# Kernel optimization log

Measured on AMD Instinct MI355X. Metric: run time of the kernel, lower is better.

## Reference

```python
import jax, jax.numpy as jnp
import numpy as np

B, T, D = 512, 200, 512

def setup_inputs() -> dict:
    key = jax.random.key(0)
    k1, k2, k3 = jax.random.split(key, 3)
    inputs = jax.random.normal(k1, (B, T, D), dtype=jnp.float32)
    # Keras 'uniform' initializer -> U(-0.05, 0.05)
    W = jax.random.uniform(k2, (T, T), minval=-0.05, maxval=0.05, dtype=jnp.float32)
    b = jax.random.uniform(k3, (T,), minval=-0.05, maxval=0.05, dtype=jnp.float32)
    return {"inputs": inputs, "W": W, "b": b}

def reference(inputs, W, b):
    # x = permute(inputs, (0,2,1)) -> [B, D, T]; scores over timestep axis
    # a = softmax(tanh(x @ W + b)) along last axis (T)
    scores = jnp.tanh(jnp.einsum('btd,ts->bds', inputs, W) + b)  # [B, D, T]
    a = jax.nn.softmax(scores, axis=-1)                           # softmax over T
    # permute back to [B, T, D], elementwise multiply, sum over T -> [B, D]
    out = jnp.einsum('bdt,btd->bd', a, inputs)
    return out
```

## Files before the change

### kernel.cpp

```cpp
#include <hip/hip_runtime.h>
#include <cstdint>
#include <cstddef>

#define B_DIM 512
#define T_DIM 200
#define D_DIM 512
#define NPAD  208
#define NKG   28
#define NT    13
#define KS_STEPS 7

typedef short  short8  __attribute__((ext_vector_type(8)));
typedef float  floatx4 __attribute__((ext_vector_type(4)));

__device__ __forceinline__ unsigned short f2bf(float f) {
  unsigned int u = __float_as_uint(f);
  u += 0x7fffu + ((u >> 16) & 1u);
  return (unsigned short)(u >> 16);
}
__device__ __forceinline__ float bf2f(unsigned short h) {
  return __uint_as_float(((unsigned int)h) << 16);
}

__global__ void prep_w_kernel(const float* __restrict__ W,
                              unsigned short* __restrict__ wf) {
  int idx = blockIdx.x * blockDim.x + threadIdx.x;
  if (idx >= NKG * 8 * NPAD) return;
  int k = idx / NPAD;
  int n = idx - k * NPAD;
  float v = (k < T_DIM && n < T_DIM) ? W[k * T_DIM + n] : 0.0f;
  wf[((size_t)(k >> 3) * NPAD + n) * 8 + (k & 7)] = f2bf(v);
}

__global__ __launch_bounds__(256, 4)
void attn_kernel(const float* __restrict__ X,
                 const unsigned short* __restrict__ wf,
                 const float* __restrict__ bias,
                 float* __restrict__ out) {
  __shared__ __align__(16) unsigned short Xa[4 * NKG * 16 * 8];

  const int tid  = threadIdx.x;
  const int wv   = tid >> 6;
  const int lane = tid & 63;
  const int l15  = lane & 15;
  const int g    = lane >> 4;

  const int gw = blockIdx.x * 4 + wv;
  const int bb = gw >> 5;
  const int d0 = (gw & 31) << 4;

  unsigned short* Xw = Xa + wv * (NKG * 16 * 8);
  const float* xbase = X + (size_t)bb * T_DIM * D_DIM + d0 + l15;

  float cur[8], nxt[8];
  {
    const float* p = xbase + (size_t)(g * 8) * D_DIM;
    #pragma unroll
    for (int j = 0; j < 8; ++j) cur[j] = p[(size_t)j * D_DIM];
  }
  #pragma unroll
  for (int ks = 0; ks < KS_STEPS; ++ks) {
    if (ks < 6) {
      if (ks < 5 || g == 0) {
        const float* p = xbase + (size_t)((ks + 1) * 32 + g * 8) * D_DIM;
        #pragma unroll
        for (int j = 0; j < 8; ++j) nxt[j] = p[(size_t)j * D_DIM];
      } else {
        #pragma unroll
        for (int j = 0; j < 8; ++j) nxt[j] = 0.0f;
      }
    }
    int4 w;
    w.x = (int)f2bf(cur[0]) | ((int)f2bf(cur[1]) << 16);
    w.y = (int)f2bf(cur[2]) | ((int)f2bf(cur[3]) << 16);
    w.z = (int)f2bf(cur[4]) | ((int)f2bf(cur[5]) << 16);
    w.w = (int)f2bf(cur[6]) | ((int)f2bf(cur[7]) << 16);
    *(int4*)&Xw[(((ks * 4 + g) * 16) + l15) * 8] = w;
    #pragma unroll
    for (int j = 0; j < 8; ++j) cur[j] = nxt[j];
  }

  floatx4 acc[NT];
  #pragma unroll
  for (int nt = 0; nt < NT; ++nt)
    acc[nt] = (floatx4){0.f, 0.f, 0.f, 0.f};

  #pragma unroll
  for (int ks = 0; ks < KS_STEPS; ++ks) {
    const int kg = ks * 4 + g;
    short8 a = *(const short8*)&Xw[((kg * 16) + l15) * 8];
    const unsigned short* wp = wf + ((size_t)kg * NPAD + l15) * 8;
    #pragma unroll
    for (int nt = 0; nt < NT; ++nt) {
      short8 bfr = *(const short8*)(wp + nt * 16 * 8);
      acc[nt] = __builtin_amdgcn_mfma_f32_16x16x32_bf16(a, bfr, acc[nt], 0, 0, 0);
    }
  }

  float part[4] = {0.f, 0.f, 0.f, 0.f};
  float rs[4]   = {0.f, 0.f, 0.f, 0.f};
  #pragma unroll
  for (int nt = 0; nt < NT; ++nt) {
    const int t = nt * 16 + l15;
    const bool valid = (t < T_DIM);
    const float bvn = valid ? bias[t] : 0.0f;
    const unsigned short* xp = &Xw[((t >> 3) * 16) * 8 + (t & 7)];
    #pragma unroll
    for (int r = 0; r < 4; ++r) {
      if (valid) {
        float z  = acc[nt][r] + bvn;
        float e  = __expf(2.0f * z);
        float th = 1.0f - __fdividef(2.0f, e + 1.0f);
        float p  = __expf(th);
        rs[r]   += p;
        const int m = g * 4 + r;
        part[r] += p * bf2f(xp[m * 8]);
      }
    }
  }
  #pragma unroll
  for (int off = 1; off <= 8; off <<= 1)
    #pragma unroll
    for (int r = 0; r < 4; ++r) {
      part[r] += __shfl_xor(part[r], off, 16);
      rs[r]   += __shfl_xor(rs[r],   off, 16);
    }

  if (l15 == 0) {
    #pragma unroll
    for (int r = 0; r < 4; ++r)
      out[(size_t)bb * D_DIM + d0 + g * 4 + r] = part[r] * __frcp_rn(rs[r]);
  }
}

extern "C" void kernel_launch(void* const* d_in, const int* in_sizes, int n_in,
                              void* d_out, int out_size, void* d_ws, size_t ws_size,
                              hipStream_t stream) {
  const float* X  = (const float*)d_in[0];
  const float* W  = (const float*)d_in[1];
  const float* bs = (const float*)d_in[2];
  float* out = (float*)d_out;
  unsigned short* wf = (unsigned short*)d_ws;

  const int wtot = NKG * 8 * NPAD;
  hipLaunchKernelGGL(prep_w_kernel, dim3((wtot + 255) / 256), dim3(256), 0, stream,
                     W, wf);
  hipLaunchKernelGGL(attn_kernel, dim3(4096), dim3(256), 0, stream,
                     X, wf, bs, out);
}
```

Baseline: 342.1 us.

## Split each 16-column tile across two waves sharing the staged X tile

Each 16-column (b, d) tile is now handled by a 128-thread block of two waves instead of one wave. The waves cooperatively stage the bf16 X tile into shared memory and split the 13 N-tiles of W between them (7 and 6). Partial softmax numerators and denominators are combined through shared memory after a block barrier. This halves per-wave MFMA and epilogue work and accumulator registers to raise parallelism and occupancy, at the cost of two __syncthreads and extra shared-memory combine traffic.

```diff
diff --git a/kernel.cpp b/kernel.cpp
--- a/kernel.cpp
+++ b/kernel.cpp
@@ -8,7 +8,6 @@
 #define NPAD  208
 #define NKG   28
 #define NT    13
-#define KS_STEPS 7
 
 typedef short  short8  __attribute__((ext_vector_type(8)));
 typedef float  floatx4 __attribute__((ext_vector_type(4)));
@@ -32,12 +31,13 @@
   wf[((size_t)(k >> 3) * NPAD + n) * 8 + (k & 7)] = f2bf(v);
 }
 
-__global__ __launch_bounds__(256, 4)
+__global__ __launch_bounds__(128, 5)
 void attn_kernel(const float* __restrict__ X,
                  const unsigned short* __restrict__ wf,
                  const float* __restrict__ bias,
                  float* __restrict__ out) {
-  __shared__ __align__(16) unsigned short Xa[4 * NKG * 16 * 8];
+  __shared__ __align__(16) unsigned short Xs[NKG * 16 * 8];
+  __shared__ float comb[2][2][16];
 
   const int tid  = threadIdx.x;
   const int wv   = tid >> 6;
@@ -45,24 +45,25 @@
   const int l15  = lane & 15;
   const int g    = lane >> 4;
 
-  const int gw = blockIdx.x * 4 + wv;
-  const int bb = gw >> 5;
-  const int d0 = (gw & 31) << 4;
+  const int bb = blockIdx.x >> 5;
+  const int d0 = (blockIdx.x & 31) << 4;
 
-  unsigned short* Xw = Xa + wv * (NKG * 16 * 8);
   const float* xbase = X + (size_t)bb * T_DIM * D_DIM + d0 + l15;
 
   float cur[8], nxt[8];
   {
-    const float* p = xbase + (size_t)(g * 8) * D_DIM;
+    const int kg = wv * 14 + g;
+    const float* p = xbase + (size_t)(kg * 8) * D_DIM;
     #pragma unroll
     for (int j = 0; j < 8; ++j) cur[j] = p[(size_t)j * D_DIM];
   }
   #pragma unroll
-  for (int ks = 0; ks < KS_STEPS; ++ks) {
-    if (ks < 6) {
-      if (ks < 5 || g == 0) {
-        const float* p = xbase + (size_t)((ks + 1) * 32 + g * 8) * D_DIM;
+  for (int s = 0; s < 4; ++s) {
+    if (s < 3) {
+      const int kg  = wv * 14 + (s + 1) * 4 + g;
+      const bool wa = ((s + 1) < 3) || (g < 2);
+      if (wa && kg < 25) {
+        const float* p = xbase + (size_t)(kg * 8) * D_DIM;
         #pragma unroll
         for (int j = 0; j < 8; ++j) nxt[j] = p[(size_t)j * D_DIM];
       } else {
@@ -70,51 +71,60 @@
         for (int j = 0; j < 8; ++j) nxt[j] = 0.0f;
       }
     }
-    int4 w;
-    w.x = (int)f2bf(cur[0]) | ((int)f2bf(cur[1]) << 16);
-    w.y = (int)f2bf(cur[2]) | ((int)f2bf(cur[3]) << 16);
-    w.z = (int)f2bf(cur[4]) | ((int)f2bf(cur[5]) << 16);
-    w.w = (int)f2bf(cur[6]) | ((int)f2bf(cur[7]) << 16);
-    *(int4*)&Xw[(((ks * 4 + g) * 16) + l15) * 8] = w;
+    const int kg  = wv * 14 + s * 4 + g;
+    const bool wa = (s < 3) || (g < 2);
+    if (wa) {
+      int4 w;
+      w.x = (int)f2bf(cur[0]) | ((int)f2bf(cur[1]) << 16);
+      w.y = (int)f2bf(cur[2]) | ((int)f2bf(cur[3]) << 16);
+      w.z = (int)f2bf(cur[4]) | ((int)f2bf(cur[5]) << 16);
+      w.w = (int)f2bf(cur[6]) | ((int)f2bf(cur[7]) << 16);
+      *(int4*)&Xs[((kg * 16) + l15) * 8] = w;
+    }
     #pragma unroll
     for (int j = 0; j < 8; ++j) cur[j] = nxt[j];
   }
+  __syncthreads();
 
-  floatx4 acc[NT];
+  const int nt0 = wv * 7;
+  const int ntc = 7 - wv;
+  floatx4 acc[7];
   #pragma unroll
-  for (int nt = 0; nt < NT; ++nt)
-    acc[nt] = (floatx4){0.f, 0.f, 0.f, 0.f};
+  for (int i = 0; i < 7; ++i) acc[i] = (floatx4){0.f, 0.f, 0.f, 0.f};
 
   #pragma unroll
-  for (int ks = 0; ks < KS_STEPS; ++ks) {
+  for (int ks = 0; ks < 7; ++ks) {
     const int kg = ks * 4 + g;
-    short8 a = *(const short8*)&Xw[((kg * 16) + l15) * 8];
-    const unsigned short* wp = wf + ((size_t)kg * NPAD + l15) * 8;
+    short8 a = *(const short8*)&Xs[((kg * 16) + l15) * 8];
+    const unsigned short* wp = wf + ((size_t)kg * NPAD + nt0 * 16 + l15) * 8;
     #pragma unroll
-    for (int nt = 0; nt < NT; ++nt) {
-      short8 bfr = *(const short8*)(wp + nt * 16 * 8);
-      acc[nt] = __builtin_amdgcn_mfma_f32_16x16x32_bf16(a, bfr, acc[nt], 0, 0, 0);
+    for (int i = 0; i < 7; ++i) {
+      if (i < ntc) {
+        short8 bfr = *(const short8*)(wp + i * 16 * 8);
+        acc[i] = __builtin_amdgcn_mfma_f32_16x16x32_bf16(a, bfr, acc[i], 0, 0, 0);
+      }
     }
   }
 
   float part[4] = {0.f, 0.f, 0.f, 0.f};
   float rs[4]   = {0.f, 0.f, 0.f, 0.f};
   #pragma unroll
-  for (int nt = 0; nt < NT; ++nt) {
-    const int t = nt * 16 + l15;
-    const bool valid = (t < T_DIM);
-    const float bvn = valid ? bias[t] : 0.0f;
-    const unsigned short* xp = &Xw[((t >> 3) * 16) * 8 + (t & 7)];
-    #pragma unroll
-    for (int r = 0; r < 4; ++r) {
-      if (valid) {
-        float z  = acc[nt][r] + bvn;
-        float e  = __expf(2.0f * z);
-        float th = 1.0f - __fdividef(2.0f, e + 1.0f);
-        float p  = __expf(th);
-        rs[r]   += p;
-        const int m = g * 4 + r;
-        part[r] += p * bf2f(xp[m * 8]);
+  for (int i = 0; i < 7; ++i) {
+    if (i < ntc) {
+      const int t = (nt0 + i) * 16 + l15;
+      const bool valid = (t < T_DIM);
+      const float bvn = valid ? bias[t] : 0.0f;
+      const unsigned short* xp = &Xs[((t >> 3) * 16) * 8 + (t & 7)];
+      #pragma unroll
+      for (int r = 0; r < 4; ++r) {
+        if (valid) {
+          float z  = acc[i][r] + bvn;
+          float e  = __expf(2.0f * z);
+          float th = 1.0f - __fdividef(2.0f, e + 1.0f);
+          float p  = __expf(th);
+          rs[r]   += p;
+          part[r] += p * bf2f(xp[(g * 4 + r) * 8]);
+        }
       }
     }
   }
@@ -128,8 +138,17 @@
 
   if (l15 == 0) {
     #pragma unroll
-    for (int r = 0; r < 4; ++r)
-      out[(size_t)bb * D_DIM + d0 + g * 4 + r] = part[r] * __frcp_rn(rs[r]);
+    for (int r = 0; r < 4; ++r) {
+      comb[wv][0][g * 4 + r] = rs[r];
+      comb[wv][1][g * 4 + r] = part[r];
+    }
+  }
+  __syncthreads();
+
+  if (wv == 0 && lane < 16) {
+    float rsum = comb[0][0][lane] + comb[1][0][lane];
+    float psum = comb[0][1][lane] + comb[1][1][lane];
+    out[(size_t)bb * D_DIM + d0 + lane] = psum * __frcp_rn(rsum);
   }
 }
 
@@ -145,6 +164,6 @@
   const int wtot = NKG * 8 * NPAD;
   hipLaunchKernelGGL(prep_w_kernel, dim3((wtot + 255) / 256), dim3(256), 0, stream,
                      W, wf);
-  hipLaunchKernelGGL(attn_kernel, dim3(4096), dim3(256), 0, stream,
+  hipLaunchKernelGGL(attn_kernel, dim3(B_DIM * 32), dim3(128), 0, stream,
                      X, wf, bs, out);
 }
```

After: 353.7 us. +3.4%, slower.
